# Kernel tuning notes

Hardware: AMD Instinct MI355X
Metric: run time of the kernel (lower is better)

The kernel has to match this reference:

```python
import jax, jax.numpy as jnp
import numpy as np

N, D, S, P = 768, 64, 32, 4
RBF_START, RBF_END = 0.0, 12.0
ENERGY_SCALE = 1.0


def setup_inputs() -> dict:
    key = jax.random.key(0)
    k = jax.random.split(key, 4)
    hid = jax.random.normal(k[0], (N, D), jnp.float32)
    # coords spread out so pairwise distances span the RBF range [0, 12]
    coords = jax.random.normal(k[1], (P, N, 3), jnp.float32) * 4.0
    W_rbf = jax.random.normal(k[2], (D, D, S), jnp.float32) / D
    b_rbf = jax.random.normal(k[3], (S,), jnp.float32) * 0.01
    weight = jnp.ones((1,), jnp.float32)
    bias = jnp.zeros((1,), jnp.float32)
    return {"hid": hid, "coords": coords, "W_rbf": W_rbf, "b_rbf": b_rbf,
            "weight": weight, "bias": bias}


def reference(hid, coords, W_rbf, b_rbf, weight, bias):
    # --- interaction matrix: einsum('xi,yj->xyij') + Linear(D*D -> S), fused ---
    # identical math to reshape(N,N,D*D) @ W.reshape(D*D,S) + b
    inter = jnp.einsum('xi,yj,ijs->xys', hid, hid, W_rbf) + b_rbf  # [N,N,S]

    # --- cdist_diff: pairwise euclidean distances per pose ---
    diff = coords[:, :, None, :] - coords[:, None, :, :]           # [P,N,N,3]
    dists = jnp.sqrt(jnp.sum(diff * diff, axis=-1) + 1e-12)        # [P,N,N]

    # --- rbf_encode: gaussian basis over [RBF_START, RBF_END] with S steps ---
    mu = jnp.linspace(RBF_START, RBF_END, S, dtype=jnp.float32)    # [S]
    sigma = (RBF_END - RBF_START) / S
    rbfs = jnp.exp(-((dists[..., None] - mu) ** 2) / (2.0 * sigma * sigma))  # [P,N,N,S]

    # --- masked interaction energy (exclude self-pairs) ---
    inv_ident = (~jnp.eye(N, dtype=bool))[None, :, :, None]        # [1,N,N,1]
    interact = inter[None] * rbfs * ENERGY_SCALE
    interact = jnp.where(inv_ident, interact, 0.0)
    U = interact.mean(axis=(-3, -2, -1)) * weight[0] + bias[0]     # [P]
    return U
```

## Files before the change

### kernel.cpp

```cpp
#include <hip/hip_runtime.h>
#include <hip/hip_bf16.h>
#include <math.h>

#define NN 768
#define DD 64
#define SS 32
#define PP 4

#define MU_STEP   (12.0f / 31.0f)
#define INV2SIG2  3.55555555555f
#define NEG2C     (-INV2SIG2 * 1.4426950408889634f)

typedef __attribute__((ext_vector_type(8))) short bf16x8;
typedef __attribute__((ext_vector_type(4))) float f32x4;

__device__ __forceinline__ unsigned short f2bf(float f) {
    unsigned u = __float_as_uint(f);
    u += 0x7FFFu + ((u >> 16) & 1u);
    return (unsigned short)(u >> 16);
}
__device__ __forceinline__ float bf2f(unsigned short b) {
    return __uint_as_float(((unsigned)b) << 16);
}

__global__ __launch_bounds__(256) void k1_T(const float* __restrict__ hid,
                                            const float* __restrict__ W,
                                            float* __restrict__ T,
                                            unsigned short* __restrict__ hbHi,
                                            unsigned short* __restrict__ hbLo,
                                            unsigned* __restrict__ ctr) {
    const int b   = blockIdx.x;
    const int tid = threadIdx.x;
    if (b == 0 && tid == 0) *ctr = 0u;

    __shared__ float hs[16 * 64];

    if (b < 192) {
        const int cb  = b & 3;
        const int xb  = b >> 2;
        const int c0  = cb * 512;
        const int x0  = xb * 16;
        const int ct  = tid & 63;
        const int xt  = tid >> 6;

        {
            const float4 v = *reinterpret_cast<const float4*>(&hid[(size_t)x0 * 64 + tid * 4]);
            *reinterpret_cast<float4*>(&hs[tid * 4]) = v;
        }
        __syncthreads();

        float acc[4][8];
#pragma unroll
        for (int m = 0; m < 4; ++m)
#pragma unroll
            for (int u = 0; u < 8; ++u) acc[m][u] = 0.0f;

        const int cbase = c0 + ct * 8;
#pragma unroll 4
        for (int i = 0; i < 64; ++i) {
            const float4 w0 = *reinterpret_cast<const float4*>(&W[(size_t)i * 2048 + cbase]);
            const float4 w1 = *reinterpret_cast<const float4*>(&W[(size_t)i * 2048 + cbase + 4]);
#pragma unroll
            for (int m = 0; m < 4; ++m) {
                const float hm = hs[(xt * 4 + m) * 64 + i];
                acc[m][0] += hm * w0.x; acc[m][1] += hm * w0.y;
                acc[m][2] += hm * w0.z; acc[m][3] += hm * w0.w;
                acc[m][4] += hm * w1.x; acc[m][5] += hm * w1.y;
                acc[m][6] += hm * w1.z; acc[m][7] += hm * w1.w;
            }
        }

#pragma unroll
        for (int m = 0; m < 4; ++m) {
            const int x = x0 + xt * 4 + m;
            float4 o0, o1;
            o0.x = acc[m][0]; o0.y = acc[m][1]; o0.z = acc[m][2]; o0.w = acc[m][3];
            o1.x = acc[m][4]; o1.y = acc[m][5]; o1.z = acc[m][6]; o1.w = acc[m][7];
            *reinterpret_cast<float4*>(&T[(size_t)x * 2048 + cbase])     = o0;
            *reinterpret_cast<float4*>(&T[(size_t)x * 2048 + cbase + 4]) = o1;
        }
    } else {
        const int base = (b - 192) * 4096 + tid * 16;
        const int y  = base >> 6;
        const int j0 = base & 63;
        const int t  = y >> 4;
        const int r  = y & 15;
        float hv[16];
#pragma unroll
        for (int c = 0; c < 4; ++c) {
            const float4 v = *reinterpret_cast<const float4*>(&hid[(size_t)y * 64 + j0 + c * 4]);
            hv[c * 4 + 0] = v.x; hv[c * 4 + 1] = v.y; hv[c * 4 + 2] = v.z; hv[c * 4 + 3] = v.w;
        }
#pragma unroll
        for (int n = 0; n < 16; ++n) {
            const int j  = j0 + n;
            const int kh = j >> 5;
            const int g  = (j >> 3) & 3;
            const int e  = j & 7;
            const int idx = t * 1024 + kh * 512 + (g * 16 + r) * 8 + e;
            const unsigned short hi = f2bf(hv[n]);
            const float lo = hv[n] - bf2f(hi);
            hbHi[idx] = hi;
            hbLo[idx] = f2bf(lo);
        }
    }
}

__global__ __launch_bounds__(256, 4) void k2_main(const float* __restrict__ coords,
                                                  const float* __restrict__ b_rbf,
                                                  const float* __restrict__ Tg,
                                                  const unsigned short* __restrict__ hbHi,
                                                  const unsigned short* __restrict__ hbLo,
                                                  float* __restrict__ partials,
                                                  unsigned* __restrict__ ctr,
                                                  const float* __restrict__ weight,
                                                  const float* __restrict__ bias_,
                                                  float* __restrict__ out) {
    const int x   = blockIdx.x;
    const int tid = threadIdx.x;
    const int l   = tid & 63;
    const int wv  = tid >> 6;
    const int g   = l >> 4;
    const int c16 = l & 15;

    __shared__ float d_s[PP][NN];
    __shared__ float c_s[PP][NN];
    __shared__ unsigned short bh_s[2048];
    __shared__ unsigned short bl_s[2048];
    __shared__ float red16[16];
    __shared__ unsigned flagS;

#pragma unroll
    for (int p = 0; p < PP; ++p) {
        const float cxx = coords[((size_t)p * NN + x) * 3 + 0];
        const float cxy = coords[((size_t)p * NN + x) * 3 + 1];
        const float cxz = coords[((size_t)p * NN + x) * 3 + 2];
#pragma unroll
        for (int yb = 0; yb < 3; ++yb) {
            const int y = yb * 256 + tid;
            const float dx = cxx - coords[((size_t)p * NN + y) * 3 + 0];
            const float dy = cxy - coords[((size_t)p * NN + y) * 3 + 1];
            const float dz = cxz - coords[((size_t)p * NN + y) * 3 + 2];
            const float d2 = fmaf(dx, dx, fmaf(dy, dy, fmaf(dz, dz, 1e-12f)));
            d_s[p][y] = sqrtf(d2);
            c_s[p][y] = d2 * NEG2C;
        }
    }

    {
        const int st = tid >> 7;
        const int kh = (tid >> 6) & 1;
        const int fl = tid & 63;
        const int jb = kh * 32 + (fl >> 4) * 8;
        const int s  = st * 16 + (fl & 15);
#pragma unroll
        for (int e = 0; e < 8; ++e) {
            const float tv = Tg[(size_t)x * 2048 + (size_t)(jb + e) * 32 + s];
            const unsigned short hi = f2bf(tv);
            const float lo = tv - bf2f(hi);
            bh_s[tid * 8 + e] = hi;
            bl_s[tid * 8 + e] = f2bf(lo);
        }
    }
    __syncthreads();

    const bf16x8 bH00 = *reinterpret_cast<const bf16x8*>(&bh_s[(0 * 64 + l) * 8]);
    const bf16x8 bH01 = *reinterpret_cast<const bf16x8*>(&bh_s[(1 * 64 + l) * 8]);
    const bf16x8 bH10 = *reinterpret_cast<const bf16x8*>(&bh_s[(2 * 64 + l) * 8]);
    const bf16x8 bH11 = *reinterpret_cast<const bf16x8*>(&bh_s[(3 * 64 + l) * 8]);
    const bf16x8 bL00 = *reinterpret_cast<const bf16x8*>(&bl_s[(0 * 64 + l) * 8]);
    const bf16x8 bL01 = *reinterpret_cast<const bf16x8*>(&bl_s[(1 * 64 + l) * 8]);
    const bf16x8 bL10 = *reinterpret_cast<const bf16x8*>(&bl_s[(2 * 64 + l) * 8]);
    const bf16x8 bL11 = *reinterpret_cast<const bf16x8*>(&bl_s[(3 * 64 + l) * 8]);

    const float mu0 = (float)(c16)      * MU_STEP;
    const float mu1 = (float)(16 + c16) * MU_STEP;
    const float A0 = -2.0f * NEG2C * mu0, B0 = NEG2C * mu0 * mu0;
    const float A1 = -2.0f * NEG2C * mu1, B1 = NEG2C * mu1 * mu1;
    const float brbf0 = b_rbf[c16];
    const float brbf1 = b_rbf[16 + c16];

    float eA[PP] = {0, 0, 0, 0};
    float eB[PP] = {0, 0, 0, 0};

    for (int k = 0; k < 12; ++k) {
        const int t  = (k << 2) + wv;
        const int ab = t * 1024 + l * 8;

        const bf16x8 aH0 = *reinterpret_cast<const bf16x8*>(&hbHi[ab]);
        const bf16x8 aH1 = *reinterpret_cast<const bf16x8*>(&hbHi[ab + 512]);
        const bf16x8 aL0 = *reinterpret_cast<const bf16x8*>(&hbLo[ab]);
        const bf16x8 aL1 = *reinterpret_cast<const bf16x8*>(&hbLo[ab + 512]);

        f32x4 acc0 = {0.0f, 0.0f, 0.0f, 0.0f};
        f32x4 acc1 = {0.0f, 0.0f, 0.0f, 0.0f};
        acc0 = __builtin_amdgcn_mfma_f32_16x16x32_bf16(aH0, bH00, acc0, 0, 0, 0);
        acc1 = __builtin_amdgcn_mfma_f32_16x16x32_bf16(aH0, bH10, acc1, 0, 0, 0);
        acc0 = __builtin_amdgcn_mfma_f32_16x16x32_bf16(aH1, bH01, acc0, 0, 0, 0);
        acc1 = __builtin_amdgcn_mfma_f32_16x16x32_bf16(aH1, bH11, acc1, 0, 0, 0);
        acc0 = __builtin_amdgcn_mfma_f32_16x16x32_bf16(aH0, bL00, acc0, 0, 0, 0);
        acc1 = __builtin_amdgcn_mfma_f32_16x16x32_bf16(aH0, bL10, acc1, 0, 0, 0);
        acc0 = __builtin_amdgcn_mfma_f32_16x16x32_bf16(aH1, bL01, acc0, 0, 0, 0);
        acc1 = __builtin_amdgcn_mfma_f32_16x16x32_bf16(aH1, bL11, acc1, 0, 0, 0);
        acc0 = __builtin_amdgcn_mfma_f32_16x16x32_bf16(aL0, bH00, acc0, 0, 0, 0);
        acc1 = __builtin_amdgcn_mfma_f32_16x16x32_bf16(aL0, bH10, acc1, 0, 0, 0);
        acc0 = __builtin_amdgcn_mfma_f32_16x16x32_bf16(aL1, bH01, acc0, 0, 0, 0);
        acc1 = __builtin_amdgcn_mfma_f32_16x16x32_bf16(aL1, bH11, acc1, 0, 0, 0);

        const int yb = t * 16 + g * 4;
        const float ab00 = acc0[0] + brbf0, ab01 = acc0[1] + brbf0,
                    ab02 = acc0[2] + brbf0, ab03 = acc0[3] + brbf0;
        const float ab10 = acc1[0] + brbf1, ab11 = acc1[1] + brbf1,
                    ab12 = acc1[2] + brbf1, ab13 = acc1[3] + brbf1;

#pragma unroll
        for (int p = 0; p < PP; ++p) {
            const f32x4 dd = *reinterpret_cast<const f32x4*>(&d_s[p][yb]);
            const f32x4 cc = *reinterpret_cast<const f32x4*>(&c_s[p][yb]);
#pragma unroll
            for (int r = 0; r < 4; ++r) {
                if (yb + r == x) continue;
                const float d  = dd[r];
                const float c0v = cc[r] + B0;
                const float c1v = cc[r] + B1;
                const float w0 = __builtin_exp2f(fmaf(A0, d, c0v));
                const float w1 = __builtin_exp2f(fmaf(A1, d, c1v));
                const float a0 = (r == 0) ? ab00 : (r == 1) ? ab01 : (r == 2) ? ab02 : ab03;
                const float a1 = (r == 0) ? ab10 : (r == 1) ? ab11 : (r == 2) ? ab12 : ab13;
                eA[p] = fmaf(a0, w0, eA[p]);
                eB[p] = fmaf(a1, w1, eB[p]);
            }
        }
    }

    float e[PP];
#pragma unroll
    for (int p = 0; p < PP; ++p) e[p] = eA[p] + eB[p];
#pragma unroll
    for (int off = 1; off < 64; off <<= 1)
#pragma unroll
        for (int p = 0; p < PP; ++p) e[p] += __shfl_xor(e[p], off, 64);

    if (l == 0) {
#pragma unroll
        for (int p = 0; p < PP; ++p) red16[wv * 4 + p] = e[p];
    }
    __syncthreads();
    if (tid < 4) {
        const float s = red16[0 * 4 + tid] + red16[1 * 4 + tid] +
                        red16[2 * 4 + tid] + red16[3 * 4 + tid];
        partials[(size_t)x * 4 + tid] = s;
    }

    __threadfence();
    __syncthreads();
    if (tid == 0) {
        const unsigned old = atomicAdd(ctr, 1u);
        flagS = (old == NN - 1) ? 1u : 0u;
    }
    __syncthreads();
    if (flagS) {
        __threadfence();
        const int p    = tid >> 6;
        const int lane = tid & 63;
        float s = 0.0f;
#pragma unroll
        for (int kk = 0; kk < 12; ++kk)
            s += partials[(size_t)(lane * 12 + kk) * 4 + p];
#pragma unroll
        for (int off = 1; off < 64; off <<= 1) s += __shfl_xor(s, off, 64);
        if (lane == 0)
            out[p] = s * (1.0f / 18874368.0f) * weight[0] + bias_[0];
    }
}

__global__ __launch_bounds__(256, 4) void k2_fb(const float* __restrict__ hid,
                                                const float* __restrict__ coords,
                                                const float* __restrict__ W,
                                                const float* __restrict__ b_rbf,
                                                float* __restrict__ partials) {
    const int x   = blockIdx.x;
    const int tid = threadIdx.x;
    const int ty  = tid & 63;
    const int ts  = tid >> 6;

    __shared__ float pool[2048 + 64 * 128];
    float* T_l = pool;
    float* h_t = pool + 2048;

    {
        float a0[4] = {0, 0, 0, 0}, a1[4] = {0, 0, 0, 0};
        for (int i = 0; i < 64; ++i) {
            const float hv = hid[(size_t)x * 64 + i];
            const float4 w0 = *reinterpret_cast<const float4*>(&W[(size_t)i * 2048 + tid * 4]);
            const float4 w1 = *reinterpret_cast<const float4*>(&W[(size_t)i * 2048 + 1024 + tid * 4]);
            a0[0] += hv * w0.x; a0[1] += hv * w0.y; a0[2] += hv * w0.z; a0[3] += hv * w0.w;
            a1[0] += hv * w1.x; a1[1] += hv * w1.y; a1[2] += hv * w1.z; a1[3] += hv * w1.w;
        }
        T_l[tid * 4 + 0] = a0[0]; T_l[tid * 4 + 1] = a0[1];
        T_l[tid * 4 + 2] = a0[2]; T_l[tid * 4 + 3] = a0[3];
        T_l[1024 + tid * 4 + 0] = a1[0]; T_l[1024 + tid * 4 + 1] = a1[1];
        T_l[1024 + tid * 4 + 2] = a1[2]; T_l[1024 + tid * 4 + 3] = a1[3];
    }

    float mu_reg[8], b_reg[8];
#pragma unroll
    for (int u = 0; u < 8; ++u) {
        const int s = ts * 8 + u;
        mu_reg[u] = (float)s * MU_STEP;
        b_reg[u]  = b_rbf[s];
    }
    float cx[PP][3];
#pragma unroll
    for (int p = 0; p < PP; ++p)
#pragma unroll
        for (int c = 0; c < 3; ++c)
            cx[p][c] = coords[(size_t)p * NN * 3 + (size_t)x * 3 + c];

    float e[PP] = {0.0f, 0.0f, 0.0f, 0.0f};
    const int srow = tid >> 1;
    const int r0   = (tid & 1) * 8;
    const int hoff = ty * 2;
    const int toff = ts * 8;

    for (int ch = 0; ch < 6; ++ch) {
        const int y0 = ch * 128;
        __syncthreads();
        {
            const int y = y0 + srow;
#pragma unroll
            for (int r = 0; r < 8; ++r) {
                const float4 v = *reinterpret_cast<const float4*>(
                    &hid[(size_t)y * 64 + (r0 + r) * 4]);
                const int j = (r0 + r) * 4;
                h_t[(j + 0) * 128 + srow] = v.x;
                h_t[(j + 1) * 128 + srow] = v.y;
                h_t[(j + 2) * 128 + srow] = v.z;
                h_t[(j + 3) * 128 + srow] = v.w;
            }
        }
        __syncthreads();

        float acc[2][8];
#pragma unroll
        for (int i = 0; i < 2; ++i)
#pragma unroll
            for (int u = 0; u < 8; ++u) acc[i][u] = 0.0f;

#pragma unroll 4
        for (int j = 0; j < 64; ++j) {
            const float h0 = h_t[j * 128 + hoff];
            const float h1 = h_t[j * 128 + hoff + 1];
            const float4 t0 = *reinterpret_cast<const float4*>(&T_l[j * 32 + toff]);
            const float4 t1 = *reinterpret_cast<const float4*>(&T_l[j * 32 + toff + 4]);
            acc[0][0] += h0 * t0.x; acc[0][1] += h0 * t0.y; acc[0][2] += h0 * t0.z; acc[0][3] += h0 * t0.w;
            acc[0][4] += h0 * t1.x; acc[0][5] += h0 * t1.y; acc[0][6] += h0 * t1.z; acc[0][7] += h0 * t1.w;
            acc[1][0] += h1 * t0.x; acc[1][1] += h1 * t0.y; acc[1][2] += h1 * t0.z; acc[1][3] += h1 * t0.w;
            acc[1][4] += h1 * t1.x; acc[1][5] += h1 * t1.y; acc[1][6] += h1 * t1.z; acc[1][7] += h1 * t1.w;
        }

        float ab[2][8];
#pragma unroll
        for (int i = 0; i < 2; ++i)
#pragma unroll
            for (int u = 0; u < 8; ++u) ab[i][u] = acc[i][u] + b_reg[u];

#pragma unroll
        for (int i = 0; i < 2; ++i) {
            const int y = y0 + hoff + i;
            if (y == x) continue;
#pragma unroll
            for (int p = 0; p < PP; ++p) {
                const float dx = cx[p][0] - coords[(size_t)p * NN * 3 + (size_t)y * 3 + 0];
                const float dy = cx[p][1] - coords[(size_t)p * NN * 3 + (size_t)y * 3 + 1];
                const float dz = cx[p][2] - coords[(size_t)p * NN * 3 + (size_t)y * 3 + 2];
                const float d  = sqrtf(dx * dx + dy * dy + dz * dz + 1e-12f);
                float ep = 0.0f;
#pragma unroll
                for (int u = 0; u < 8; ++u) {
                    const float t = d - mu_reg[u];
                    const float w = __builtin_exp2f(t * t * NEG2C);
                    ep = fmaf(ab[i][u], w, ep);
                }
                e[p] += ep;
            }
        }
    }

#pragma unroll
    for (int off = 1; off < 64; off <<= 1)
#pragma unroll
        for (int p = 0; p < PP; ++p) e[p] += __shfl_xor(e[p], off, 64);

    __syncthreads();
    if (ty == 0) {
#pragma unroll
        for (int p = 0; p < PP; ++p) pool[ts * 4 + p] = e[p];
    }
    __syncthreads();
    if (tid < 4) {
        const float s = pool[0 * 4 + tid] + pool[1 * 4 + tid] +
                        pool[2 * 4 + tid] + pool[3 * 4 + tid];
        partials[(size_t)x * 4 + tid] = s;
    }
}

__global__ __launch_bounds__(256) void k3_final(const float* __restrict__ partials,
                                                const float* __restrict__ weight,
                                                const float* __restrict__ bias_,
                                                float* __restrict__ out) {
    const int p    = threadIdx.x >> 6;
    const int lane = threadIdx.x & 63;
    float s = 0.0f;
#pragma unroll
    for (int k = 0; k < 12; ++k) s += partials[(size_t)(lane * 12 + k) * 4 + p];
#pragma unroll
    for (int off = 1; off < 64; off <<= 1) s += __shfl_xor(s, off, 64);
    if (lane == 0)
        out[p] = s * (1.0f / 18874368.0f) * weight[0] + bias_[0];
}

extern "C" void kernel_launch(void* const* d_in, const int* in_sizes, int n_in,
                              void* d_out, int out_size, void* d_ws, size_t ws_size,
                              hipStream_t stream) {
    const float* hid    = (const float*)d_in[0];
    const float* coords = (const float*)d_in[1];
    const float* W      = (const float*)d_in[2];
    const float* b_rbf  = (const float*)d_in[3];
    const float* weight = (const float*)d_in[4];
    const float* bias_  = (const float*)d_in[5];
    float* out = (float*)d_out;

    const size_t T_BYTES    = (size_t)NN * 2048 * sizeof(float);
    const size_t HB_BYTES   = (size_t)48 * 1024 * sizeof(unsigned short);
    const size_t PART_BYTES = (size_t)NN * 4 * sizeof(float);
    const bool use_ws = ws_size >= T_BYTES + 2 * HB_BYTES + PART_BYTES + 64;

    float*          Tg       = (float*)d_ws;
    unsigned short* hbHi     = (unsigned short*)((char*)d_ws + T_BYTES);
    unsigned short* hbLo     = (unsigned short*)((char*)d_ws + T_BYTES + HB_BYTES);
    float*          partials = use_ws ? (float*)((char*)d_ws + T_BYTES + 2 * HB_BYTES)
                                      : (float*)d_ws;
    unsigned*       ctr      = (unsigned*)((char*)d_ws + T_BYTES + 2 * HB_BYTES + PART_BYTES);

    if (use_ws) {
        k1_T<<<204, 256, 0, stream>>>(hid, W, Tg, hbHi, hbLo, ctr);
        k2_main<<<NN, 256, 0, stream>>>(coords, b_rbf, Tg, hbHi, hbLo, partials,
                                        ctr, weight, bias_, out);
    } else {
        k2_fb<<<NN, 256, 0, stream>>>(hid, coords, W, b_rbf, partials);
        k3_final<<<1, 256, 0, stream>>>(partials, weight, bias_, out);
    }
}
```

Before: 91.17 us.

## Precompute pairwise distances in separate kernel and split main kernel per row into halves

Adds a kernel that writes all pose distance matrices to a global workspace, so the main kernel no longer builds distance and coefficient tables in shared memory. The main kernel now launches two blocks per row, each covering half the y tiles, with higher occupancy bounds and a rewritten, vectorized T load into shared memory. The intent is more parallelism and less shared memory per block. In exchange it adds an extra launch plus a 9 MB global round trip for distances, and B fragments are reloaded from LDS every iteration.

```diff
diff --git a/kernel.cpp b/kernel.cpp
--- a/kernel.cpp
+++ b/kernel.cpp
@@ -6,6 +6,7 @@
 #define DD 64
 #define SS 32
 #define PP 4
+#define NB2 1536
 
 #define MU_STEP   (12.0f / 31.0f)
 #define INV2SIG2  3.55555555555f
@@ -23,15 +24,34 @@
     return __uint_as_float(((unsigned)b) << 16);
 }
 
+__global__ __launch_bounds__(256) void kD(const float* __restrict__ coords,
+                                          float* __restrict__ dG,
+                                          unsigned* __restrict__ ctr) {
+    const int b = blockIdx.x;
+    if (b == 0 && threadIdx.x == 0) *ctr = 0u;
+    const int p = b / NN;
+    const int x = b - p * NN;
+    const float cxx = coords[((size_t)p * NN + x) * 3 + 0];
+    const float cxy = coords[((size_t)p * NN + x) * 3 + 1];
+    const float cxz = coords[((size_t)p * NN + x) * 3 + 2];
+#pragma unroll
+    for (int yb = 0; yb < 3; ++yb) {
+        const int y = yb * 256 + threadIdx.x;
+        const float dx = cxx - coords[((size_t)p * NN + y) * 3 + 0];
+        const float dy = cxy - coords[((size_t)p * NN + y) * 3 + 1];
+        const float dz = cxz - coords[((size_t)p * NN + y) * 3 + 2];
+        dG[((size_t)p * NN + x) * NN + y] =
+            sqrtf(fmaf(dx, dx, fmaf(dy, dy, fmaf(dz, dz, 1e-12f))));
+    }
+}
+
 __global__ __launch_bounds__(256) void k1_T(const float* __restrict__ hid,
                                             const float* __restrict__ W,
                                             float* __restrict__ T,
                                             unsigned short* __restrict__ hbHi,
-                                            unsigned short* __restrict__ hbLo,
-                                            unsigned* __restrict__ ctr) {
+                                            unsigned short* __restrict__ hbLo) {
     const int b   = blockIdx.x;
     const int tid = threadIdx.x;
-    if (b == 0 && tid == 0) *ctr = 0u;
 
     __shared__ float hs[16 * 64];
 
@@ -106,91 +126,79 @@
     }
 }
 
-__global__ __launch_bounds__(256, 4) void k2_main(const float* __restrict__ coords,
-                                                  const float* __restrict__ b_rbf,
+__global__ __launch_bounds__(256, 6) void k2_main(const float* __restrict__ b_rbf,
                                                   const float* __restrict__ Tg,
                                                   const unsigned short* __restrict__ hbHi,
                                                   const unsigned short* __restrict__ hbLo,
+                                                  const float* __restrict__ dG,
                                                   float* __restrict__ partials,
                                                   unsigned* __restrict__ ctr,
                                                   const float* __restrict__ weight,
                                                   const float* __restrict__ bias_,
                                                   float* __restrict__ out) {
-    const int x   = blockIdx.x;
+    const int bid = blockIdx.x;
+    const int x   = bid >> 1;
+    const int h   = bid & 1;
     const int tid = threadIdx.x;
     const int l   = tid & 63;
     const int wv  = tid >> 6;
     const int g   = l >> 4;
     const int c16 = l & 15;
 
-    __shared__ float d_s[PP][NN];
-    __shared__ float c_s[PP][NN];
     __shared__ unsigned short bh_s[2048];
     __shared__ unsigned short bl_s[2048];
     __shared__ float red16[16];
     __shared__ unsigned flagS;
 
-#pragma unroll
-    for (int p = 0; p < PP; ++p) {
-        const float cxx = coords[((size_t)p * NN + x) * 3 + 0];
-        const float cxy = coords[((size_t)p * NN + x) * 3 + 1];
-        const float cxz = coords[((size_t)p * NN + x) * 3 + 2];
-#pragma unroll
-        for (int yb = 0; yb < 3; ++yb) {
-            const int y = yb * 256 + tid;
-            const float dx = cxx - coords[((size_t)p * NN + y) * 3 + 0];
-            const float dy = cxy - coords[((size_t)p * NN + y) * 3 + 1];
-            const float dz = cxz - coords[((size_t)p * NN + y) * 3 + 2];
-            const float d2 = fmaf(dx, dx, fmaf(dy, dy, fmaf(dz, dz, 1e-12f)));
-            d_s[p][y] = sqrtf(d2);
-            c_s[p][y] = d2 * NEG2C;
-        }
-    }
-
     {
-        const int st = tid >> 7;
-        const int kh = (tid >> 6) & 1;
-        const int fl = tid & 63;
-        const int jb = kh * 32 + (fl >> 4) * 8;
-        const int s  = st * 16 + (fl & 15);
-#pragma unroll
-        for (int e = 0; e < 8; ++e) {
-            const float tv = Tg[(size_t)x * 2048 + (size_t)(jb + e) * 32 + s];
-            const unsigned short hi = f2bf(tv);
-            const float lo = tv - bf2f(hi);
-            bh_s[tid * 8 + e] = hi;
-            bl_s[tid * 8 + e] = f2bf(lo);
-        }
-    }
-    __syncthreads();
-
-    const bf16x8 bH00 = *reinterpret_cast<const bf16x8*>(&bh_s[(0 * 64 + l) * 8]);
-    const bf16x8 bH01 = *reinterpret_cast<const bf16x8*>(&bh_s[(1 * 64 + l) * 8]);
-    const bf16x8 bH10 = *reinterpret_cast<const bf16x8*>(&bh_s[(2 * 64 + l) * 8]);
-    const bf16x8 bH11 = *reinterpret_cast<const bf16x8*>(&bh_s[(3 * 64 + l) * 8]);
-    const bf16x8 bL00 = *reinterpret_cast<const bf16x8*>(&bl_s[(0 * 64 + l) * 8]);
-    const bf16x8 bL01 = *reinterpret_cast<const bf16x8*>(&bl_s[(1 * 64 + l) * 8]);
-    const bf16x8 bL10 = *reinterpret_cast<const bf16x8*>(&bl_s[(2 * 64 + l) * 8]);
-    const bf16x8 bL11 = *reinterpret_cast<const bf16x8*>(&bl_s[(3 * 64 + l) * 8]);
+        const float4 t0 = *reinterpret_cast<const float4*>(&Tg[(size_t)x * 2048 + tid * 8]);
+        const float4 t1 = *reinterpret_cast<const float4*>(&Tg[(size_t)x * 2048 + tid * 8 + 4]);
+        float tv[8];
+        tv[0] = t0.x; tv[1] = t0.y; tv[2] = t0.z; tv[3] = t0.w;
+        tv[4] = t1.x; tv[5] = t1.y; tv[6] = t1.z; tv[7] = t1.w;
+        const int j    = tid >> 2;
+        const int kh   = tid >> 7;
+        const int jg   = (tid >> 5) & 3;
+        const int e    = j & 7;
+        const int st   = (tid >> 1) & 1;
+        const int srb  = (tid & 1) * 8;
+        const int base = (st * 2 + kh) * 512 + (jg * 16 + srb) * 8 + e;
+#pragma unroll
+        for (int q = 0; q < 8; ++q) {
+            const unsigned short hi = f2bf(tv[q]);
+            const float lo = tv[q] - bf2f(hi);
+            bh_s[base + q * 8] = hi;
+            bl_s[base + q * 8] = f2bf(lo);
+        }
+    }
+    __syncthreads();
 
     const float mu0 = (float)(c16)      * MU_STEP;
     const float mu1 = (float)(16 + c16) * MU_STEP;
-    const float A0 = -2.0f * NEG2C * mu0, B0 = NEG2C * mu0 * mu0;
-    const float A1 = -2.0f * NEG2C * mu1, B1 = NEG2C * mu1 * mu1;
+    const float A0 = -2.0f * NEG2C * mu0, B0v = NEG2C * mu0 * mu0;
+    const float A1 = -2.0f * NEG2C * mu1, B1v = NEG2C * mu1 * mu1;
     const float brbf0 = b_rbf[c16];
     const float brbf1 = b_rbf[16 + c16];
 
-    float eA[PP] = {0, 0, 0, 0};
-    float eB[PP] = {0, 0, 0, 0};
-
-    for (int k = 0; k < 12; ++k) {
-        const int t  = (k << 2) + wv;
+    float e0 = 0.0f, e1 = 0.0f, e2 = 0.0f, e3 = 0.0f;
+
+    for (int k = 0; k < 6; ++k) {
+        const int t  = h * 24 + (k << 2) + wv;
         const int ab = t * 1024 + l * 8;
 
         const bf16x8 aH0 = *reinterpret_cast<const bf16x8*>(&hbHi[ab]);
         const bf16x8 aH1 = *reinterpret_cast<const bf16x8*>(&hbHi[ab + 512]);
         const bf16x8 aL0 = *reinterpret_cast<const bf16x8*>(&hbLo[ab]);
         const bf16x8 aL1 = *reinterpret_cast<const bf16x8*>(&hbLo[ab + 512]);
+
+        const bf16x8 bH00 = *reinterpret_cast<const bf16x8*>(&bh_s[l * 8]);
+        const bf16x8 bH01 = *reinterpret_cast<const bf16x8*>(&bh_s[512 + l * 8]);
+        const bf16x8 bH10 = *reinterpret_cast<const bf16x8*>(&bh_s[1024 + l * 8]);
+        const bf16x8 bH11 = *reinterpret_cast<const bf16x8*>(&bh_s[1536 + l * 8]);
+        const bf16x8 bL00 = *reinterpret_cast<const bf16x8*>(&bl_s[l * 8]);
+        const bf16x8 bL01 = *reinterpret_cast<const bf16x8*>(&bl_s[512 + l * 8]);
+        const bf16x8 bL10 = *reinterpret_cast<const bf16x8*>(&bl_s[1024 + l * 8]);
+        const bf16x8 bL11 = *reinterpret_cast<const bf16x8*>(&bl_s[1536 + l * 8]);
 
         f32x4 acc0 = {0.0f, 0.0f, 0.0f, 0.0f};
         f32x4 acc1 = {0.0f, 0.0f, 0.0f, 0.0f};
@@ -212,30 +220,31 @@
                     ab02 = acc0[2] + brbf0, ab03 = acc0[3] + brbf0;
         const float ab10 = acc1[0] + brbf1, ab11 = acc1[1] + brbf1,
                     ab12 = acc1[2] + brbf1, ab13 = acc1[3] + brbf1;
+        const size_t dbase = (size_t)x * NN + yb;
 
 #pragma unroll
         for (int p = 0; p < PP; ++p) {
-            const f32x4 dd = *reinterpret_cast<const f32x4*>(&d_s[p][yb]);
-            const f32x4 cc = *reinterpret_cast<const f32x4*>(&c_s[p][yb]);
+            const float4 dd = *reinterpret_cast<const float4*>(
+                &dG[(size_t)p * NN * NN + dbase]);
+            float* ep = (p == 0) ? &e0 : (p == 1) ? &e1 : (p == 2) ? &e2 : &e3;
+            float accp = 0.0f;
 #pragma unroll
             for (int r = 0; r < 4; ++r) {
                 if (yb + r == x) continue;
-                const float d  = dd[r];
-                const float c0v = cc[r] + B0;
-                const float c1v = cc[r] + B1;
-                const float w0 = __builtin_exp2f(fmaf(A0, d, c0v));
-                const float w1 = __builtin_exp2f(fmaf(A1, d, c1v));
+                const float d   = (r == 0) ? dd.x : (r == 1) ? dd.y : (r == 2) ? dd.z : dd.w;
+                const float d2c = d * d * NEG2C;
+                const float w0 = __builtin_exp2f(fmaf(A0, d, d2c + B0v));
+                const float w1 = __builtin_exp2f(fmaf(A1, d, d2c + B1v));
                 const float a0 = (r == 0) ? ab00 : (r == 1) ? ab01 : (r == 2) ? ab02 : ab03;
                 const float a1 = (r == 0) ? ab10 : (r == 1) ? ab11 : (r == 2) ? ab12 : ab13;
-                eA[p] = fmaf(a0, w0, eA[p]);
-                eB[p] = fmaf(a1, w1, eB[p]);
+                accp = fmaf(a0, w0, accp);
+                accp = fmaf(a1, w1, accp);
             }
-        }
-    }
-
-    float e[PP];
-#pragma unroll
-    for (int p = 0; p < PP; ++p) e[p] = eA[p] + eB[p];
+            *ep += accp;
+        }
+    }
+
+    float e[PP] = {e0, e1, e2, e3};
 #pragma unroll
     for (int off = 1; off < 64; off <<= 1)
 #pragma unroll
@@ -249,14 +258,14 @@
     if (tid < 4) {
         const float s = red16[0 * 4 + tid] + red16[1 * 4 + tid] +
                         red16[2 * 4 + tid] + red16[3 * 4 + tid];
-        partials[(size_t)x * 4 + tid] = s;
+        partials[(size_t)bid * 4 + tid] = s;
     }
 
     __threadfence();
     __syncthreads();
     if (tid == 0) {
         const unsigned old = atomicAdd(ctr, 1u);
-        flagS = (old == NN - 1) ? 1u : 0u;
+        flagS = (old == NB2 - 1) ? 1u : 0u;
     }
     __syncthreads();
     if (flagS) {
@@ -265,8 +274,8 @@
         const int lane = tid & 63;
         float s = 0.0f;
 #pragma unroll
-        for (int kk = 0; kk < 12; ++kk)
-            s += partials[(size_t)(lane * 12 + kk) * 4 + p];
+        for (int kk = 0; kk < 24; ++kk)
+            s += partials[(size_t)(lane * 24 + kk) * 4 + p];
 #pragma unroll
         for (int off = 1; off < 64; off <<= 1) s += __shfl_xor(s, off, 64);
         if (lane == 0)
@@ -433,20 +442,25 @@
 
     const size_t T_BYTES    = (size_t)NN * 2048 * sizeof(float);
     const size_t HB_BYTES   = (size_t)48 * 1024 * sizeof(unsigned short);
-    const size_t PART_BYTES = (size_t)NN * 4 * sizeof(float);
-    const bool use_ws = ws_size >= T_BYTES + 2 * HB_BYTES + PART_BYTES + 64;
-
-    float*          Tg       = (float*)d_ws;
-    unsigned short* hbHi     = (unsigned short*)((char*)d_ws + T_BYTES);
-    unsigned short* hbLo     = (unsigned short*)((char*)d_ws + T_BYTES + HB_BYTES);
-    float*          partials = use_ws ? (float*)((char*)d_ws + T_BYTES + 2 * HB_BYTES)
+    const size_t D_BYTES    = (size_t)PP * NN * NN * sizeof(float);
+    const size_t PART_BYTES = (size_t)NB2 * 4 * sizeof(float);
+    const size_t TOTAL = T_BYTES + 2 * HB_BYTES + D_BYTES + PART_BYTES + 64;
+    const bool use_ws = ws_size >= TOTAL;
+
+    char* w = (char*)d_ws;
+    float*          Tg       = (float*)w;
+    unsigned short* hbHi     = (unsigned short*)(w + T_BYTES);
+    unsigned short* hbLo     = (unsigned short*)(w + T_BYTES + HB_BYTES);
+    float*          dG       = (float*)(w + T_BYTES + 2 * HB_BYTES);
+    float*          partials = use_ws ? (float*)(w + T_BYTES + 2 * HB_BYTES + D_BYTES)
                                       : (float*)d_ws;
-    unsigned*       ctr      = (unsigned*)((char*)d_ws + T_BYTES + 2 * HB_BYTES + PART_BYTES);
+    unsigned*       ctr      = (unsigned*)(w + T_BYTES + 2 * HB_BYTES + D_BYTES + PART_BYTES);
 
     if (use_ws) {
-        k1_T<<<204, 256, 0, stream>>>(hid, W, Tg, hbHi, hbLo, ctr);
-        k2_main<<<NN, 256, 0, stream>>>(coords, b_rbf, Tg, hbHi, hbLo, partials,
-                                        ctr, weight, bias_, out);
+        kD<<<PP * NN, 256, 0, stream>>>(coords, dG, ctr);
+        k1_T<<<204, 256, 0, stream>>>(hid, W, Tg, hbHi, hbLo);
+        k2_main<<<NB2, 256, 0, stream>>>(b_rbf, Tg, hbHi, hbLo, dG, partials,
+                                         ctr, weight, bias_, out);
     } else {
         k2_fb<<<NN, 256, 0, stream>>>(hid, coords, W, b_rbf, partials);
         k3_final<<<1, 256, 0, stream>>>(partials, weight, bias_, out);
```

Result: slower. 174.8 us (+91.7%).
